# Optimization experiments

Hardware: AMD Instinct MI355X
Metric: run time of the kernel (lower is better)

Reference implementation:

```python
import jax, jax.numpy as jnp
import numpy as np

DIM = 128
EDGE_FEAT_DIM = 2
N_NODES = 50000
N_EDGES = 600000
EPS = 1e-5


def setup_inputs() -> dict:
    key = jax.random.key(0)
    ks = jax.random.split(key, 16)
    d = DIM
    inp = {}
    inp["x"] = jax.random.normal(ks[0], (N_NODES, d), dtype=jnp.float32)
    inp["edge_index"] = jax.random.randint(ks[1], (2, N_EDGES), 0, N_NODES, dtype=jnp.int32)
    inp["edge_weight_norm"] = jax.random.uniform(ks[2], (N_EDGES,), dtype=jnp.float32)
    inp["edge_feat"] = jax.random.normal(ks[3], (N_EDGES, EDGE_FEAT_DIM), dtype=jnp.float32)
    inp["batch"] = jnp.zeros((N_NODES,), dtype=jnp.int32)
    # phi: Linear(dim, dim)
    inp["W_phi"] = jax.random.normal(ks[4], (d, d), dtype=jnp.float32) * (1.0 / np.sqrt(d))
    inp["b_phi"] = jnp.zeros((d,), dtype=jnp.float32)
    # edge_gate: Linear(2d+2, d) -> BN(d) -> GELU -> Linear(d, 1)
    din = 2 * d + EDGE_FEAT_DIM
    inp["W_g1"] = jax.random.normal(ks[5], (din, d), dtype=jnp.float32) * (1.0 / np.sqrt(din))
    inp["b_g1"] = jnp.zeros((d,), dtype=jnp.float32)
    inp["bn_gamma"] = jnp.ones((d,), dtype=jnp.float32)
    inp["bn_beta"] = jnp.zeros((d,), dtype=jnp.float32)
    inp["bn_mean"] = jnp.zeros((d,), dtype=jnp.float32)
    inp["bn_var"] = jnp.ones((d,), dtype=jnp.float32)
    inp["W_g2"] = jax.random.normal(ks[6], (d, 1), dtype=jnp.float32) * (1.0 / np.sqrt(d))
    inp["b_g2"] = jnp.zeros((1,), dtype=jnp.float32)
    # upd: Linear(2d, d)
    inp["W_u"] = jax.random.normal(ks[7], (2 * d, d), dtype=jnp.float32) * (1.0 / np.sqrt(2 * d))
    inp["b_u"] = jnp.zeros((d,), dtype=jnp.float32)
    # LayerNorm(dim)
    inp["ln_gamma"] = jnp.ones((d,), dtype=jnp.float32)
    inp["ln_beta"] = jnp.zeros((d,), dtype=jnp.float32)
    return inp


def reference(x, edge_index, edge_weight_norm, edge_feat, batch,
              W_phi, b_phi, W_g1, b_g1, bn_gamma, bn_beta, bn_mean, bn_var,
              W_g2, b_g2, W_u, b_u, ln_gamma, ln_beta):
    src, dst = edge_index[0], edge_index[1]
    # phi(x): [N, d]
    xj = x @ W_phi + b_phi
    # edge gate MLP on [x_dst, x_src, e]: [E, 2d+2]
    g_in = jnp.concatenate([x[dst], x[src], edge_feat], axis=-1)
    h1 = g_in @ W_g1 + b_g1
    h1 = (h1 - bn_mean) * jax.lax.rsqrt(bn_var + EPS) * bn_gamma + bn_beta  # BN eval mode
    h1 = jax.nn.gelu(h1, approximate=False)
    gate = jax.nn.sigmoid(h1 @ W_g2 + b_g2)[:, 0]  # [E]
    # messages and scatter-add aggregation
    msg = xj[src] * (edge_weight_norm * gate)[:, None]  # [E, d]
    agg = jax.ops.segment_sum(msg, dst, num_segments=x.shape[0])  # [N, d]
    # update MLP + GELU + residual + LayerNorm
    h = jnp.concatenate([x, agg], axis=-1) @ W_u + b_u
    h = jax.nn.gelu(h, approximate=False)
    y = x + h
    mu = jnp.mean(y, axis=-1, keepdims=True)
    var = jnp.var(y, axis=-1, keepdims=True)
    return (y - mu) * jax.lax.rsqrt(var + EPS) * ln_gamma + ln_beta
```

## Files before the change

### kernel.cpp

```cpp
#include <hip/hip_runtime.h>
#include <hip/hip_fp16.h>
#include <math.h>

#define DIM 128
#define NN 50000
#define NE 600000
#define EPS 1e-5f
#define CAP 64

struct H8 { __half2 h[4]; };
struct F8 { float4 a, b; };

typedef _Float16 f16x8 __attribute__((ext_vector_type(8)));
typedef float    f32x4 __attribute__((ext_vector_type(4)));

__device__ __forceinline__ float gelu_fast(float x) {
    const float c1 = 2.3022085f;
    const float c2 = 0.1029437f;
    const float x2 = x * x;
    const float z  = x * __builtin_fmaf(c2, x2, c1);
    const float u  = __builtin_amdgcn_exp2f(z);
    const float r  = __builtin_amdgcn_rcpf(1.f + u);
    return __builtin_fmaf(-x, r, x);
}

__device__ __forceinline__ float sigmoid_fast(float y) {
    const float u = __builtin_amdgcn_exp2f(-1.4426950409f * y);
    return __builtin_amdgcn_rcpf(1.f + u);
}

__global__ __launch_bounds__(256) void k_prep_scale(
    const float* __restrict__ Wg1, const float* __restrict__ bg1,
    const float* __restrict__ bng, const float* __restrict__ bnb,
    const float* __restrict__ bnm, const float* __restrict__ bnv,
    __half* __restrict__ WABth, float* __restrict__ bA,
    float* __restrict__ w0p, float* __restrict__ w1p)
{
    const int k = blockIdx.x;
    const int t = threadIdx.x;
    const int c = t & 127;
    const float s = bng[c] * rsqrtf(bnv[c] + EPS);
    const float w = (t < 128) ? Wg1[k * DIM + c] : Wg1[(DIM + k) * DIM + c];
    WABth[t * DIM + k] = __float2half(w * s);
    if (k == 0 && t < 128) {
        const float tt = bnb[c] - bnm[c] * s;
        bA[c]  = bg1[c] * s + tt;
        w0p[c] = Wg1[256 * DIM + c] * s;
        w1p[c] = Wg1[257 * DIM + c] * s;
    }
}

__global__ __launch_bounds__(128) void k_prep_wpu(
    const float* __restrict__ Wphi, const float* __restrict__ bphi,
    const float* __restrict__ Wu,
    __half* __restrict__ Wct, float* __restrict__ bpu)
{
    const int a = blockIdx.x;
    const int j = threadIdx.x;
    float acc = 0.f;
    #pragma unroll 8
    for (int k = 0; k < DIM; ++k)
        acc += Wphi[a * DIM + k] * Wu[(DIM + k) * DIM + j];
    Wct[j * 256 + a]       = __float2half(Wu[a * DIM + j]);
    Wct[j * 256 + 128 + a] = __float2half(acc);
    if (a == 0) {
        float b = 0.f;
        #pragma unroll 8
        for (int k = 0; k < DIM; ++k)
            b += bphi[k] * Wu[(DIM + k) * DIM + j];
        bpu[j] = b;
    }
}

__global__ __launch_bounds__(256) void k_node_mfma(
    const float* __restrict__ x, const __half* __restrict__ WABth,
    const float* __restrict__ bA,
    __half* __restrict__ A, __half* __restrict__ Bv, __half* __restrict__ xh)
{
    __shared__ __half tile[64][264];
    const int t    = threadIdx.x;
    const int wv   = t >> 6;
    const int lane = t & 63;
    const int n16  = lane & 15;
    const int quad = lane >> 4;
    const int m0   = blockIdx.x * 64;

    f32x4 acc[4][4];
    #pragma unroll
    for (int mt = 0; mt < 4; ++mt)
        #pragma unroll
        for (int nt = 0; nt < 4; ++nt)
            acc[mt][nt] = (f32x4){0.f, 0.f, 0.f, 0.f};

    int rowm[4];
    #pragma unroll
    for (int mt = 0; mt < 4; ++mt)
        rowm[mt] = min(m0 + mt * 16 + n16, NN - 1);

    #pragma unroll
    for (int ks = 0; ks < 4; ++ks) {
        const int ko = ks * 32 + quad * 8;
        f16x8 bf[4];
        #pragma unroll
        for (int nt = 0; nt < 4; ++nt) {
            const int c = wv * 64 + nt * 16 + n16;
            bf[nt] = *(const f16x8*)(WABth + c * DIM + ko);
        }
        #pragma unroll
        for (int mt = 0; mt < 4; ++mt) {
            const float4 xa = *(const float4*)(x + (size_t)rowm[mt] * DIM + ko);
            const float4 xb = *(const float4*)(x + (size_t)rowm[mt] * DIM + ko + 4);
            f16x8 af;
            af[0] = (_Float16)xa.x; af[1] = (_Float16)xa.y;
            af[2] = (_Float16)xa.z; af[3] = (_Float16)xa.w;
            af[4] = (_Float16)xb.x; af[5] = (_Float16)xb.y;
            af[6] = (_Float16)xb.z; af[7] = (_Float16)xb.w;
            if (wv == 0)
                *(f16x8*)(xh + (size_t)rowm[mt] * DIM + ko) = af;
            #pragma unroll
            for (int nt = 0; nt < 4; ++nt)
                acc[mt][nt] = __builtin_amdgcn_mfma_f32_16x16x32_f16(
                    af, bf[nt], acc[mt][nt], 0, 0, 0);
        }
    }

    #pragma unroll
    for (int nt = 0; nt < 4; ++nt) {
        const int c = wv * 64 + nt * 16 + n16;
        const float bias = (c < 128) ? bA[c] : 0.f;
        #pragma unroll
        for (int mt = 0; mt < 4; ++mt)
            #pragma unroll
            for (int reg = 0; reg < 4; ++reg)
                tile[mt * 16 + quad * 4 + reg][c] =
                    __float2half(acc[mt][nt][reg] + bias);
    }
    __syncthreads();

    #pragma unroll
    for (int i = 0; i < 8; ++i) {
        const int chunk = t + i * 256;
        const int row = chunk >> 5;
        const int o   = (chunk & 31) * 8;
        if (m0 + row < NN) {
            const uint4 v = *(const uint4*)&tile[row][o];
            if (o < 128) *(uint4*)(A  + (size_t)(m0 + row) * DIM + o)       = v;
            else         *(uint4*)(Bv + (size_t)(m0 + row) * DIM + o - 128) = v;
        }
    }
}

__global__ __launch_bounds__(256) void k_gate(
    const int*   __restrict__ ei,  const float* __restrict__ ew,
    const float* __restrict__ ef,
    const __half* __restrict__ A,  const __half* __restrict__ Bv,
    const float* __restrict__ w0p, const float* __restrict__ w1p,
    const float* __restrict__ Wg2, const float* __restrict__ bg2,
    int* __restrict__ deg, int2* __restrict__ pairs)
{
    const int t    = threadIdx.x;
    const int lane = t & 63;
    const int sub  = lane >> 4;
    const int sl   = lane & 15;
    const int c8   = sl * 8;
    const int e0   = (blockIdx.x * 4 + (t >> 6)) * 8 + sub * 2;

    const F8 WG = *(const F8*)(Wg2 + c8);
    const F8 W0 = *(const F8*)(w0p + c8);
    const F8 W1 = *(const F8*)(w1p + c8);
    const float bg2v = bg2[0];
    const float* w0 = (const float*)&W0;
    const float* w1 = (const float*)&W1;
    const float* wg = (const float*)&WG;

    const int2   srcs = *(const int2*)(ei + e0);
    const int2   dsts = *(const int2*)(ei + NE + e0);
    const float4 efv  = *(const float4*)(ef + 2 * e0);
    const float2 ewv  = *(const float2*)(ew + e0);

    const H8 a0 = *(const H8*)(A  + (size_t)dsts.x * DIM + c8);
    const H8 b0 = *(const H8*)(Bv + (size_t)srcs.x * DIM + c8);
    const H8 a1 = *(const H8*)(A  + (size_t)dsts.y * DIM + c8);
    const H8 b1 = *(const H8*)(Bv + (size_t)srcs.y * DIM + c8);

    float p0 = 0.f, p1 = 0.f;
    #pragma unroll
    for (int i = 0; i < 4; ++i) {
        const float2 s0 = __half22float2(__hadd2(a0.h[i], b0.h[i]));
        const float2 s1 = __half22float2(__hadd2(a1.h[i], b1.h[i]));
        const int c0 = 2 * i, c1 = 2 * i + 1;
        float h;
        h = s0.x + efv.x * w0[c0] + efv.y * w1[c0];
        p0 = __builtin_fmaf(gelu_fast(h), wg[c0], p0);
        h = s0.y + efv.x * w0[c1] + efv.y * w1[c1];
        p0 = __builtin_fmaf(gelu_fast(h), wg[c1], p0);
        h = s1.x + efv.z * w0[c0] + efv.w * w1[c0];
        p1 = __builtin_fmaf(gelu_fast(h), wg[c0], p1);
        h = s1.y + efv.z * w0[c1] + efv.w * w1[c1];
        p1 = __builtin_fmaf(gelu_fast(h), wg[c1], p1);
    }
    #pragma unroll
    for (int off = 1; off < 16; off <<= 1) {
        p0 += __shfl_xor(p0, off, 64);
        p1 += __shfl_xor(p1, off, 64);
    }

    if (sl == 0) {
        const float coef0 = ewv.x * sigmoid_fast(p0 + bg2v);
        const float coef1 = ewv.y * sigmoid_fast(p1 + bg2v);
        const int pos0 = atomicAdd(&deg[dsts.x], 1);
        if (pos0 < CAP)
            pairs[(size_t)dsts.x * CAP + pos0] = make_int2(srcs.x, __float_as_int(coef0));
        const int pos1 = atomicAdd(&deg[dsts.y], 1);
        if (pos1 < CAP)
            pairs[(size_t)dsts.y * CAP + pos1] = make_int2(srcs.y, __float_as_int(coef1));
    }
}

__global__ __launch_bounds__(256) void k_agg(
    const int* __restrict__ deg, const int2* __restrict__ pairs,
    const __half* __restrict__ xh,
    __half* __restrict__ aggh, float* __restrict__ sc)
{
    const int t    = threadIdx.x;
    const int lane = t & 63;
    const int sub  = lane >> 4;
    const int sl   = lane & 15;
    const int c8   = sl * 8;
    const int n    = (blockIdx.x * 4 + (t >> 6)) * 4 + sub;
    const int d    = min(deg[n], CAP);

    float acc[8];
    #pragma unroll
    for (int i = 0; i < 8; ++i) acc[i] = 0.f;
    float scn = 0.f;

    for (int j = 0; j < d; ++j) {
        const int2 pr = pairs[(size_t)n * CAP + j];
        const float cf = __int_as_float(pr.y);
        const H8 xv = *(const H8*)(xh + (size_t)pr.x * DIM + c8);
        #pragma unroll
        for (int i = 0; i < 4; ++i) {
            const float2 xf = __half22float2(xv.h[i]);
            acc[2 * i]     = __builtin_fmaf(cf, xf.x, acc[2 * i]);
            acc[2 * i + 1] = __builtin_fmaf(cf, xf.y, acc[2 * i + 1]);
        }
        scn += cf;
    }

    H8 hv;
    #pragma unroll
    for (int i = 0; i < 4; ++i) {
        hv.h[i].x = __float2half_rn(acc[2 * i]);
        hv.h[i].y = __float2half_rn(acc[2 * i + 1]);
    }
    *(H8*)(aggh + (size_t)n * DIM + c8) = hv;
    if (sl == 0) sc[n] = scn;
}

__global__ __launch_bounds__(256) void k_update_mfma(
    const __half* __restrict__ xh, const __half* __restrict__ aggh,
    const __half* __restrict__ Wct,
    const float* __restrict__ sc,
    const float* __restrict__ bu, const float* __restrict__ bpu,
    const float* __restrict__ lng, const float* __restrict__ lnb,
    float* __restrict__ out)
{
    const int t    = threadIdx.x;
    const int wv   = t >> 6;
    const int lane = t & 63;
    const int n16  = lane & 15;
    const int quad = lane >> 4;
    const int m0   = blockIdx.x * 64;
    const int mrow = m0 + wv * 16;
    const int arow = min(mrow + n16, NN - 1);

    f32x4 acc[8];
    #pragma unroll
    for (int nt = 0; nt < 8; ++nt) acc[nt] = (f32x4){0.f, 0.f, 0.f, 0.f};

    #pragma unroll
    for (int ks = 0; ks < 4; ++ks) {
        const int ko = ks * 32 + quad * 8;
        const f16x8 af = *(const f16x8*)(xh + (size_t)arow * DIM + ko);
        #pragma unroll
        for (int nt = 0; nt < 8; ++nt) {
            const f16x8 bf = *(const f16x8*)(Wct + (nt * 16 + n16) * 256 + ko);
            acc[nt] = __builtin_amdgcn_mfma_f32_16x16x32_f16(af, bf, acc[nt], 0, 0, 0);
        }
    }
    #pragma unroll
    for (int ks = 0; ks < 4; ++ks) {
        const int ko = ks * 32 + quad * 8;
        const f16x8 af = *(const f16x8*)(aggh + (size_t)arow * DIM + ko);
        #pragma unroll
        for (int nt = 0; nt < 8; ++nt) {
            const f16x8 bf = *(const f16x8*)(Wct + (nt * 16 + n16) * 256 + 128 + ko);
            acc[nt] = __builtin_amdgcn_mfma_f32_16x16x32_f16(af, bf, acc[nt], 0, 0, 0);
        }
    }

    int   rows[4];
    float scv[4];
    #pragma unroll
    for (int reg = 0; reg < 4; ++reg) {
        rows[reg] = mrow + quad * 4 + reg;
        scv[reg]  = sc[min(rows[reg], NN - 1)];
    }

    float yv[8][4];
    float s[4]  = {0.f, 0.f, 0.f, 0.f};
    float ss[4] = {0.f, 0.f, 0.f, 0.f};
    const float is2 = 0.70710678118654752f;

    #pragma unroll
    for (int nt = 0; nt < 8; ++nt) {
        const int c = nt * 16 + n16;
        const float buv = bu[c], bpv = bpu[c];
        #pragma unroll
        for (int reg = 0; reg < 4; ++reg) {
            float h = acc[nt][reg] + buv + scv[reg] * bpv;
            h = 0.5f * h * (1.f + erff(h * is2));
            const float xv = __half2float(xh[(size_t)min(rows[reg], NN - 1) * DIM + c]);
            const float y = xv + h;
            yv[nt][reg] = y;
            s[reg]  += y;
            ss[reg] += y * y;
        }
    }

    #pragma unroll
    for (int reg = 0; reg < 4; ++reg) {
        #pragma unroll
        for (int off = 1; off < 16; off <<= 1) {
            s[reg]  += __shfl_xor(s[reg],  off, 64);
            ss[reg] += __shfl_xor(ss[reg], off, 64);
        }
    }

    float mu[4], rs[4];
    #pragma unroll
    for (int reg = 0; reg < 4; ++reg) {
        mu[reg] = s[reg] * (1.f / DIM);
        const float var = ss[reg] * (1.f / DIM) - mu[reg] * mu[reg];
        rs[reg] = rsqrtf(var + EPS);
    }

    #pragma unroll
    for (int nt = 0; nt < 8; ++nt) {
        const int c = nt * 16 + n16;
        const float gg = lng[c], bb = lnb[c];
        #pragma unroll
        for (int reg = 0; reg < 4; ++reg) {
            if (rows[reg] < NN)
                out[(size_t)rows[reg] * DIM + c] =
                    (yv[nt][reg] - mu[reg]) * rs[reg] * gg + bb;
        }
    }
}

extern "C" void kernel_launch(void* const* d_in, const int* in_sizes, int n_in,
                              void* d_out, int out_size, void* d_ws, size_t ws_size,
                              hipStream_t stream)
{
    const float* x    = (const float*)d_in[0];
    const int*   ei   = (const int*)  d_in[1];
    const float* ew   = (const float*)d_in[2];
    const float* ef   = (const float*)d_in[3];
    const float* Wphi = (const float*)d_in[5];
    const float* bphi = (const float*)d_in[6];
    const float* Wg1  = (const float*)d_in[7];
    const float* bg1  = (const float*)d_in[8];
    const float* bng  = (const float*)d_in[9];
    const float* bnb  = (const float*)d_in[10];
    const float* bnm  = (const float*)d_in[11];
    const float* bnv  = (const float*)d_in[12];
    const float* Wg2  = (const float*)d_in[13];
    const float* bg2  = (const float*)d_in[14];
    const float* Wu   = (const float*)d_in[15];
    const float* bu   = (const float*)d_in[16];
    const float* lng  = (const float*)d_in[17];
    const float* lnb  = (const float*)d_in[18];

    float* out = (float*)d_out;

    char* wsb = (char*)d_ws;
    size_t off = 0;
    auto carve = [&](size_t bytes) -> void* {
        void* p = wsb + off;
        off += (bytes + 255) & ~(size_t)255;
        return p;
    };
    __half* xh    = (__half*)carve((size_t)NN * DIM * 2);
    __half* A     = (__half*)carve((size_t)NN * DIM * 2);
    __half* Bv    = (__half*)carve((size_t)NN * DIM * 2);
    __half* aggh  = (__half*)carve((size_t)NN * DIM * 2);
    __half* WABth = (__half*)carve(256 * DIM * 2);
    __half* Wct   = (__half*)carve(DIM * 256 * 2);
    float*  bA    = (float*) carve(DIM * 4);
    float*  w0p   = (float*) carve(DIM * 4);
    float*  w1p   = (float*) carve(DIM * 4);
    float*  bpu   = (float*) carve(DIM * 4);
    int*    deg   = (int*)   carve((size_t)NN * 4);
    int2*   pairs = (int2*)  carve((size_t)NN * CAP * 8);
    float*  sc    = (float*) carve((size_t)NN * 4);

    hipMemsetAsync(deg, 0, (size_t)NN * 4, stream);

    k_prep_scale<<<128, 256, 0, stream>>>(Wg1, bg1, bng, bnb, bnm, bnv,
                                          WABth, bA, w0p, w1p);
    k_prep_wpu<<<128, 128, 0, stream>>>(Wphi, bphi, Wu, Wct, bpu);
    k_node_mfma<<<(NN + 63) / 64, 256, 0, stream>>>(x, WABth, bA, A, Bv, xh);
    k_gate<<<NE / 32, 256, 0, stream>>>(ei, ew, ef, A, Bv, w0p, w1p, Wg2, bg2,
                                        deg, pairs);
    k_agg<<<NN / 16, 256, 0, stream>>>(deg, pairs, xh, aggh, sc);
    k_update_mfma<<<(NN + 63) / 64, 256, 0, stream>>>(xh, aggh, Wct, sc,
                                                      bu, bpu, lng, lnb, out);
}
```

Measured before the change: 294.2 us.

## Fuse neighbor aggregation into update MFMA kernel via shared-memory tiles

Merges the aggregation kernel into the update GEMM kernel. Each block gathers the 64 rows' neighbor sums into LDS along with its x tile, then runs the MFMA update and LayerNorm directly from shared memory. This drops the aggh and sc round-trips through global memory and one launch. It also unrolls the gather loop by two for more loads in flight and swaps erff for the fast GELU approximation. In exchange, the gather now runs at 256 threads per 64 rows, which gives less parallelism than the separate aggregation kernel had, and the approximate GELU adds numerical error.

```diff
diff --git a/kernel.cpp b/kernel.cpp
--- a/kernel.cpp
+++ b/kernel.cpp
@@ -217,101 +217,126 @@
     }
 }
 
-__global__ __launch_bounds__(256) void k_agg(
+__global__ __launch_bounds__(256) void k_agg_update(
     const int* __restrict__ deg, const int2* __restrict__ pairs,
-    const __half* __restrict__ xh,
-    __half* __restrict__ aggh, float* __restrict__ sc)
-{
-    const int t    = threadIdx.x;
-    const int lane = t & 63;
-    const int sub  = lane >> 4;
-    const int sl   = lane & 15;
-    const int c8   = sl * 8;
-    const int n    = (blockIdx.x * 4 + (t >> 6)) * 4 + sub;
-    const int d    = min(deg[n], CAP);
-
-    float acc[8];
-    #pragma unroll
-    for (int i = 0; i < 8; ++i) acc[i] = 0.f;
-    float scn = 0.f;
-
-    for (int j = 0; j < d; ++j) {
-        const int2 pr = pairs[(size_t)n * CAP + j];
-        const float cf = __int_as_float(pr.y);
-        const H8 xv = *(const H8*)(xh + (size_t)pr.x * DIM + c8);
-        #pragma unroll
-        for (int i = 0; i < 4; ++i) {
-            const float2 xf = __half22float2(xv.h[i]);
-            acc[2 * i]     = __builtin_fmaf(cf, xf.x, acc[2 * i]);
-            acc[2 * i + 1] = __builtin_fmaf(cf, xf.y, acc[2 * i + 1]);
-        }
-        scn += cf;
-    }
-
-    H8 hv;
-    #pragma unroll
-    for (int i = 0; i < 4; ++i) {
-        hv.h[i].x = __float2half_rn(acc[2 * i]);
-        hv.h[i].y = __float2half_rn(acc[2 * i + 1]);
-    }
-    *(H8*)(aggh + (size_t)n * DIM + c8) = hv;
-    if (sl == 0) sc[n] = scn;
-}
-
-__global__ __launch_bounds__(256) void k_update_mfma(
-    const __half* __restrict__ xh, const __half* __restrict__ aggh,
-    const __half* __restrict__ Wct,
-    const float* __restrict__ sc,
+    const __half* __restrict__ xh, const __half* __restrict__ Wct,
     const float* __restrict__ bu, const float* __restrict__ bpu,
     const float* __restrict__ lng, const float* __restrict__ lnb,
     float* __restrict__ out)
 {
+    __shared__ __half xt[64][136];
+    __shared__ __half at[64][136];
+    __shared__ float sct[64];
+
     const int t    = threadIdx.x;
     const int wv   = t >> 6;
     const int lane = t & 63;
     const int n16  = lane & 15;
     const int quad = lane >> 4;
     const int m0   = blockIdx.x * 64;
-    const int mrow = m0 + wv * 16;
-    const int arow = min(mrow + n16, NN - 1);
-
-    f32x4 acc[8];
-    #pragma unroll
-    for (int nt = 0; nt < 8; ++nt) acc[nt] = (f32x4){0.f, 0.f, 0.f, 0.f};
-
+
+    #pragma unroll
+    for (int i = 0; i < 4; ++i) {
+        const int idx = i * 256 + t;
+        const int row = idx >> 4;
+        const int col = (idx & 15) * 8;
+        const int grow = min(m0 + row, NN - 1);
+        *(f16x8*)&xt[row][col] = *(const f16x8*)(xh + (size_t)grow * DIM + col);
+    }
+
+    const int slot = t >> 4;
+    const int sl   = t & 15;
+    const int c8   = sl * 8;
+
+    #pragma unroll
+    for (int r = 0; r < 4; ++r) {
+        const int lr = r * 16 + slot;
+        const int nc = min(m0 + lr, NN - 1);
+        const int d  = min(deg[nc], CAP);
+        const size_t base = (size_t)nc * CAP;
+
+        float acc[8];
+        #pragma unroll
+        for (int i = 0; i < 8; ++i) acc[i] = 0.f;
+        float scn = 0.f;
+
+        int j = 0;
+        for (; j + 1 < d; j += 2) {
+            const int2 pr0 = pairs[base + j];
+            const int2 pr1 = pairs[base + j + 1];
+            const float cf0 = __int_as_float(pr0.y);
+            const float cf1 = __int_as_float(pr1.y);
+            const H8 xv0 = *(const H8*)(xh + (size_t)pr0.x * DIM + c8);
+            const H8 xv1 = *(const H8*)(xh + (size_t)pr1.x * DIM + c8);
+            #pragma unroll
+            for (int i = 0; i < 4; ++i) {
+                const float2 f0 = __half22float2(xv0.h[i]);
+                const float2 f1 = __half22float2(xv1.h[i]);
+                acc[2 * i]     = __builtin_fmaf(cf0, f0.x, acc[2 * i]);
+                acc[2 * i + 1] = __builtin_fmaf(cf0, f0.y, acc[2 * i + 1]);
+                acc[2 * i]     = __builtin_fmaf(cf1, f1.x, acc[2 * i]);
+                acc[2 * i + 1] = __builtin_fmaf(cf1, f1.y, acc[2 * i + 1]);
+            }
+            scn += cf0 + cf1;
+        }
+        if (j < d) {
+            const int2 pr = pairs[base + j];
+            const float cf = __int_as_float(pr.y);
+            const H8 xv = *(const H8*)(xh + (size_t)pr.x * DIM + c8);
+            #pragma unroll
+            for (int i = 0; i < 4; ++i) {
+                const float2 f = __half22float2(xv.h[i]);
+                acc[2 * i]     = __builtin_fmaf(cf, f.x, acc[2 * i]);
+                acc[2 * i + 1] = __builtin_fmaf(cf, f.y, acc[2 * i + 1]);
+            }
+            scn += cf;
+        }
+
+        f16x8 hv;
+        #pragma unroll
+        for (int i = 0; i < 8; ++i) hv[i] = (_Float16)acc[i];
+        *(f16x8*)&at[lr][c8] = hv;
+        if (sl == 0) sct[lr] = scn;
+    }
+    __syncthreads();
+
+    f32x4 acc2[8];
+    #pragma unroll
+    for (int nt = 0; nt < 8; ++nt) acc2[nt] = (f32x4){0.f, 0.f, 0.f, 0.f};
+
+    const int rloc = wv * 16 + n16;
     #pragma unroll
     for (int ks = 0; ks < 4; ++ks) {
         const int ko = ks * 32 + quad * 8;
-        const f16x8 af = *(const f16x8*)(xh + (size_t)arow * DIM + ko);
+        const f16x8 af = *(const f16x8*)&xt[rloc][ko];
         #pragma unroll
         for (int nt = 0; nt < 8; ++nt) {
             const f16x8 bf = *(const f16x8*)(Wct + (nt * 16 + n16) * 256 + ko);
-            acc[nt] = __builtin_amdgcn_mfma_f32_16x16x32_f16(af, bf, acc[nt], 0, 0, 0);
+            acc2[nt] = __builtin_amdgcn_mfma_f32_16x16x32_f16(af, bf, acc2[nt], 0, 0, 0);
         }
     }
     #pragma unroll
     for (int ks = 0; ks < 4; ++ks) {
         const int ko = ks * 32 + quad * 8;
-        const f16x8 af = *(const f16x8*)(aggh + (size_t)arow * DIM + ko);
+        const f16x8 af = *(const f16x8*)&at[rloc][ko];
         #pragma unroll
         for (int nt = 0; nt < 8; ++nt) {
             const f16x8 bf = *(const f16x8*)(Wct + (nt * 16 + n16) * 256 + 128 + ko);
-            acc[nt] = __builtin_amdgcn_mfma_f32_16x16x32_f16(af, bf, acc[nt], 0, 0, 0);
-        }
-    }
-
-    int   rows[4];
+            acc2[nt] = __builtin_amdgcn_mfma_f32_16x16x32_f16(af, bf, acc2[nt], 0, 0, 0);
+        }
+    }
+
+    int   rl[4];
     float scv[4];
     #pragma unroll
     for (int reg = 0; reg < 4; ++reg) {
-        rows[reg] = mrow + quad * 4 + reg;
-        scv[reg]  = sc[min(rows[reg], NN - 1)];
+        rl[reg]  = wv * 16 + quad * 4 + reg;
+        scv[reg] = sct[rl[reg]];
     }
 
     float yv[8][4];
     float s[4]  = {0.f, 0.f, 0.f, 0.f};
     float ss[4] = {0.f, 0.f, 0.f, 0.f};
-    const float is2 = 0.70710678118654752f;
 
     #pragma unroll
     for (int nt = 0; nt < 8; ++nt) {
@@ -319,9 +344,9 @@
         const float buv = bu[c], bpv = bpu[c];
         #pragma unroll
         for (int reg = 0; reg < 4; ++reg) {
-            float h = acc[nt][reg] + buv + scv[reg] * bpv;
-            h = 0.5f * h * (1.f + erff(h * is2));
-            const float xv = __half2float(xh[(size_t)min(rows[reg], NN - 1) * DIM + c]);
+            float h = acc2[nt][reg] + buv + scv[reg] * bpv;
+            h = gelu_fast(h);
+            const float xv = __half2float(xt[rl[reg]][c]);
             const float y = xv + h;
             yv[nt][reg] = y;
             s[reg]  += y;
@@ -352,8 +377,9 @@
         const float gg = lng[c], bb = lnb[c];
         #pragma unroll
         for (int reg = 0; reg < 4; ++reg) {
-            if (rows[reg] < NN)
-                out[(size_t)rows[reg] * DIM + c] =
+            const int grow = m0 + rl[reg];
+            if (grow < NN)
+                out[(size_t)grow * DIM + c] =
                     (yv[nt][reg] - mu[reg]) * rs[reg] * gg + bb;
         }
     }
@@ -394,7 +420,6 @@
     __half* xh    = (__half*)carve((size_t)NN * DIM * 2);
     __half* A     = (__half*)carve((size_t)NN * DIM * 2);
     __half* Bv    = (__half*)carve((size_t)NN * DIM * 2);
-    __half* aggh  = (__half*)carve((size_t)NN * DIM * 2);
     __half* WABth = (__half*)carve(256 * DIM * 2);
     __half* Wct   = (__half*)carve(DIM * 256 * 2);
     float*  bA    = (float*) carve(DIM * 4);
@@ -403,7 +428,6 @@
     float*  bpu   = (float*) carve(DIM * 4);
     int*    deg   = (int*)   carve((size_t)NN * 4);
     int2*   pairs = (int2*)  carve((size_t)NN * CAP * 8);
-    float*  sc    = (float*) carve((size_t)NN * 4);
 
     hipMemsetAsync(deg, 0, (size_t)NN * 4, stream);
 
@@ -413,7 +437,6 @@
     k_node_mfma<<<(NN + 63) / 64, 256, 0, stream>>>(x, WABth, bA, A, Bv, xh);
     k_gate<<<NE / 32, 256, 0, stream>>>(ei, ew, ef, A, Bv, w0p, w1p, Wg2, bg2,
                                         deg, pairs);
-    k_agg<<<NN / 16, 256, 0, stream>>>(deg, pairs, xh, aggh, sc);
-    k_update_mfma<<<(NN + 63) / 64, 256, 0, stream>>>(xh, aggh, Wct, sc,
-                                                      bu, bpu, lng, lnb, out);
-}
+    k_agg_update<<<(NN + 63) / 64, 256, 0, stream>>>(deg, pairs, xh, Wct,
+                                                     bu, bpu, lng, lnb, out);
+}
```

After: 293.4 us. Within noise of the previous version (-0.3%).
